# Kernel optimization log

Measured on AMD Instinct MI355X. Metric: run time of the kernel, lower is better.

The kernel has to match this reference:

```python
import jax, jax.numpy as jnp
import numpy as np

N = 100000      # n_heads + n_tails (graph nodes)
E = 1600000     # nnz of sparse adjacency A_in
D = 128         # in_dim == out_dim == embed_dim
LAMDA = 0.5
ALPHA = 0.1
LAYER = 1
LN_EPS = 1e-5
LEAKY_SLOPE = 0.01


def setup_inputs() -> dict:
    key = jax.random.key(0)
    ks = jax.random.split(key, 12)
    glorot = lambda k, shape: jax.random.uniform(
        k, shape, jnp.float32, -1.0, 1.0) * np.sqrt(6.0 / (shape[0] + shape[1]))
    stdv = 1.0 / np.sqrt(D)
    return {
        "ego_embeddings": jax.random.normal(ks[0], (N, D), jnp.float32),
        "h0": jax.random.normal(ks[1], (N, D), jnp.float32),  # all_layers[0]
        "vals": jax.random.uniform(ks[2], (E,), jnp.float32),
        "row": jax.random.randint(ks[3], (E,), 0, N, jnp.int32),
        "col": jax.random.randint(ks[4], (E,), 0, N, jnp.int32),
        # nn.Parameter weight (in_dim, in_dim), uniform(-stdv, stdv)
        "weight": jax.random.uniform(ks[5], (D, D), jnp.float32, -stdv, stdv),
        # linear_h0: embed_dim -> in_dim
        "w_h0": glorot(ks[6], (D, D)),
        "b_h0": jnp.zeros((D,), jnp.float32),
        # linear: in_dim -> out_dim
        "w_lin": glorot(ks[7], (D, D)),
        "b_lin": jnp.zeros((D,), jnp.float32),
        # LayerNorm(out_dim)
        "gamma": jnp.ones((D,), jnp.float32),
        "beta_ln": jnp.zeros((D,), jnp.float32),
    }


def _layernorm(x, g, b):
    mu = jnp.mean(x, axis=-1, keepdims=True)
    var = jnp.mean(jnp.square(x - mu), axis=-1, keepdims=True)
    return (x - mu) * jax.lax.rsqrt(var + LN_EPS) * g + b


def reference(ego_embeddings, h0, vals, weight, w_h0, b_h0, w_lin, b_lin,
              gamma, beta_ln, row, col):
    n = ego_embeddings.shape[0]
    # side_embeddings = A_in @ ego_embeddings  (sparse COO SpMM)
    msgs = vals[:, None] * ego_embeddings[col]          # [E, D] gather
    side = jax.ops.segment_sum(msgs, row, num_segments=n)
    # gcn aggregator
    hi = ego_embeddings + side
    # residual_connection with identity mapping (GCNII-style)
    h0p = h0 @ w_h0.T + b_h0
    residual = (1.0 - ALPHA) * hi + ALPHA * h0p
    beta = float(np.log(LAMDA / LAYER + 1.0))
    identity_mapping = (1.0 - beta) + beta * weight     # [D, D]
    emb = residual @ identity_mapping
    # linear + LeakyReLU
    emb = jax.nn.leaky_relu(emb @ w_lin.T + b_lin, LEAKY_SLOPE)
    # LayerNorm; dropout p=0 -> identity
    return _layernorm(emb, gamma, beta_ln)
```

## Files before the change

kernel.cpp:

```cpp
#include <hip/hip_runtime.h>

#define DD 128

__global__ void hist_k(const int* __restrict__ rowi, int* __restrict__ cnt, int E) {
  int e = blockIdx.x * 256 + threadIdx.x;
  if (e < E) atomicAdd(&cnt[rowi[e]], 1);
}

__global__ __launch_bounds__(256) void scan1_k(const int* __restrict__ cnt,
                                               int* __restrict__ bsum, int n) {
  __shared__ int red[256];
  int base = blockIdx.x * 1024 + threadIdx.x * 4;
  int s = 0;
  if (base + 3 < n) {
    int4 v = *(const int4*)(cnt + base);
    s = v.x + v.y + v.z + v.w;
  } else {
#pragma unroll
    for (int j = 0; j < 4; ++j) if (base + j < n) s += cnt[base + j];
  }
  red[threadIdx.x] = s;
  __syncthreads();
#pragma unroll
  for (int off = 128; off > 0; off >>= 1) {
    if (threadIdx.x < off) red[threadIdx.x] += red[threadIdx.x + off];
    __syncthreads();
  }
  if (threadIdx.x == 0) bsum[blockIdx.x] = red[0];
}

__global__ __launch_bounds__(256) void scan2_k(int* __restrict__ bsum, int nb) {
  __shared__ int part[256];
  int t = threadIdx.x;
  int v = (t < nb) ? bsum[t] : 0;
  part[t] = v;
  __syncthreads();
#pragma unroll
  for (int off = 1; off < 256; off <<= 1) {
    int u = (t >= off) ? part[t - off] : 0;
    __syncthreads();
    part[t] += u;
    __syncthreads();
  }
  if (t < nb) bsum[t] = part[t] - v;
}

__global__ __launch_bounds__(256) void scan3_k(const int* __restrict__ cnt,
                                               const int* __restrict__ bsum,
                                               int* __restrict__ rowptr,
                                               int* __restrict__ cursor, int n, int E) {
  __shared__ int tsum[256];
  int base = blockIdx.x * 1024 + threadIdx.x * 4;
  int v0 = 0, v1 = 0, v2 = 0, v3 = 0;
  if (base + 3 < n) {
    int4 v = *(const int4*)(cnt + base);
    v0 = v.x; v1 = v.y; v2 = v.z; v3 = v.w;
  } else {
    if (base + 0 < n) v0 = cnt[base + 0];
    if (base + 1 < n) v1 = cnt[base + 1];
    if (base + 2 < n) v2 = cnt[base + 2];
    if (base + 3 < n) v3 = cnt[base + 3];
  }
  int s = v0 + v1 + v2 + v3;
  tsum[threadIdx.x] = s;
  __syncthreads();
#pragma unroll
  for (int off = 1; off < 256; off <<= 1) {
    int u = (threadIdx.x >= off) ? tsum[threadIdx.x - off] : 0;
    __syncthreads();
    tsum[threadIdx.x] += u;
    __syncthreads();
  }
  int run = bsum[blockIdx.x] + tsum[threadIdx.x] - s;
  int p1 = run + v0, p2 = p1 + v1, p3 = p2 + v2;
  if (base + 3 < n) {
    *(int4*)(rowptr + base) = (int4){run, p1, p2, p3};
    *(int4*)(cursor + base) = (int4){run, p1, p2, p3};
  } else {
    if (base + 0 < n) { rowptr[base + 0] = run; cursor[base + 0] = run; }
    if (base + 1 < n) { rowptr[base + 1] = p1;  cursor[base + 1] = p1; }
    if (base + 2 < n) { rowptr[base + 2] = p2;  cursor[base + 2] = p2; }
    if (base + 3 < n) { rowptr[base + 3] = p3;  cursor[base + 3] = p3; }
  }
  if (blockIdx.x == 0 && threadIdx.x == 0) rowptr[n] = E;
}

__global__ void scatter_k(const int* __restrict__ rowi, const int* __restrict__ coli,
                          const float* __restrict__ vals, int* __restrict__ cursor,
                          int2* __restrict__ edgeS, int E) {
  int e = blockIdx.x * 256 + threadIdx.x;
  if (e < E) {
    int r = rowi[e];
    int p = atomicAdd(&cursor[r], 1);
    edgeS[p] = make_int2(coli[e], __float_as_int(vals[e]));
  }
}

__global__ void w2_k(const float* __restrict__ weight, const float* __restrict__ w_lin,
                     float* __restrict__ W2) {
  const float BETA = 0.40546510810816438f;
  int idx = blockIdx.x * 256 + threadIdx.x;
  int i = idx >> 7, j = idx & 127;
  const float* wi = weight + i * DD;
  const float* lj = w_lin + j * DD;
  float s = 0.f;
#pragma unroll 8
  for (int k = 0; k < DD; ++k) s = fmaf(fmaf(BETA, wi[k], 1.0f - BETA), lj[k], s);
  W2[idx] = s;
}

__global__ void wt_k(const float* __restrict__ W2, const float* __restrict__ w_h0,
                     const float* __restrict__ b_h0, const float* __restrict__ b_lin,
                     float* __restrict__ Wf, float* __restrict__ cvec) {
  int idx = blockIdx.x * 256 + threadIdx.x;
  if (idx < 16384) {
    Wf[idx] = 0.9f * W2[idx];
  } else if (idx < 32768) {
    int t = idx - 16384;
    int p = t >> 7, n = t & 127;
    float s = 0.f;
#pragma unroll 8
    for (int k = 0; k < DD; ++k) s = fmaf(w_h0[k * DD + p], W2[k * DD + n], s);
    Wf[(128 + p) * DD + n] = 0.1f * s;
  } else if (idx < 32896) {
    int n = idx - 32768;
    float s = 0.f;
    for (int k = 0; k < DD; ++k) s = fmaf(b_h0[k], W2[k * DD + n], s);
    cvec[n] = fmaf(0.1f, s, b_lin[n]);
  }
}

__global__ __launch_bounds__(256) void fused_k(
    const float* __restrict__ ego, const int2* __restrict__ edgeS,
    const int* __restrict__ rowptr, const float* __restrict__ h0,
    const float* __restrict__ Wf, const float* __restrict__ cvec,
    const float* __restrict__ gamma, const float* __restrict__ betaln,
    float* __restrict__ out, int n, int E) {
  __shared__ float lds[4][2048];
  int wave = threadIdx.x >> 6;
  int lane = threadIdx.x & 63;
  int half = lane >> 5;
  int q = lane & 31;
  float* xs = &lds[wave][0];
  int row0 = blockIdx.x * 32 + wave * 8;
  const float4* eg4 = (const float4*)ego;
  const float4* h4 = (const float4*)h0;

#pragma unroll
  for (int t = 0; t < 8; ++t) {
    int r = row0 + t;
    if (r >= n) r = n - 1;
    float4 acc;
    if (half == 0) acc = eg4[(size_t)r * 32 + q];
    else           acc = (float4){0.f, 0.f, 0.f, 0.f};
    float4 hrow = h4[(size_t)r * 32 + q];
    int beg = rowptr[r], end = rowptr[r + 1];
    int e = beg;
    for (; e + 8 <= end; e += 8) {
      int2 m0 = edgeS[e + 0 + half];
      int2 m1 = edgeS[e + 2 + half];
      int2 m2 = edgeS[e + 4 + half];
      int2 m3 = edgeS[e + 6 + half];
      float4 g0 = eg4[(size_t)m0.x * 32 + q];
      float4 g1 = eg4[(size_t)m1.x * 32 + q];
      float4 g2 = eg4[(size_t)m2.x * 32 + q];
      float4 g3 = eg4[(size_t)m3.x * 32 + q];
      float v0 = __int_as_float(m0.y), v1 = __int_as_float(m1.y);
      float v2 = __int_as_float(m2.y), v3 = __int_as_float(m3.y);
      acc.x = fmaf(v0, g0.x, acc.x); acc.y = fmaf(v0, g0.y, acc.y);
      acc.z = fmaf(v0, g0.z, acc.z); acc.w = fmaf(v0, g0.w, acc.w);
      acc.x = fmaf(v1, g1.x, acc.x); acc.y = fmaf(v1, g1.y, acc.y);
      acc.z = fmaf(v1, g1.z, acc.z); acc.w = fmaf(v1, g1.w, acc.w);
      acc.x = fmaf(v2, g2.x, acc.x); acc.y = fmaf(v2, g2.y, acc.y);
      acc.z = fmaf(v2, g2.z, acc.z); acc.w = fmaf(v2, g2.w, acc.w);
      acc.x = fmaf(v3, g3.x, acc.x); acc.y = fmaf(v3, g3.y, acc.y);
      acc.z = fmaf(v3, g3.z, acc.z); acc.w = fmaf(v3, g3.w, acc.w);
    }
    for (; e < end; e += 2) {
      int idx = e + half;
      bool ok = idx < end;
      int ci = ok ? idx : (E > idx ? idx : E - 1);
      if (ci >= E) ci = E - 1;
      int2 m = edgeS[ci];
      float v = ok ? __int_as_float(m.y) : 0.f;
      float4 g = eg4[(size_t)m.x * 32 + q];
      acc.x = fmaf(v, g.x, acc.x); acc.y = fmaf(v, g.y, acc.y);
      acc.z = fmaf(v, g.z, acc.z); acc.w = fmaf(v, g.w, acc.w);
    }
    acc.x += __shfl_xor(acc.x, 32, 64);
    acc.y += __shfl_xor(acc.y, 32, 64);
    acc.z += __shfl_xor(acc.z, 32, 64);
    acc.w += __shfl_xor(acc.w, 32, 64);
    if (half == 0) *(float4*)(xs + t * 256 + 4 * q) = acc;
    else           *(float4*)(xs + t * 256 + 128 + 4 * q) = hrow;
  }

  float acc0[8], acc1[8];
#pragma unroll
  for (int r = 0; r < 8; ++r) { acc0[r] = 0.f; acc1[r] = 0.f; }

  for (int kb = 0; kb < 64; ++kb) {
    int k = kb * 4;
    float wA0 = Wf[(k + 0) * DD + lane];
    float wA1 = Wf[(k + 1) * DD + lane];
    float wA2 = Wf[(k + 2) * DD + lane];
    float wA3 = Wf[(k + 3) * DD + lane];
    float wB0 = Wf[(k + 0) * DD + 64 + lane];
    float wB1 = Wf[(k + 1) * DD + 64 + lane];
    float wB2 = Wf[(k + 2) * DD + 64 + lane];
    float wB3 = Wf[(k + 3) * DD + 64 + lane];
#pragma unroll
    for (int r = 0; r < 8; ++r) {
      float4 xv = *(const float4*)(xs + r * 256 + k);
      acc0[r] = fmaf(xv.x, wA0, acc0[r]);
      acc0[r] = fmaf(xv.y, wA1, acc0[r]);
      acc0[r] = fmaf(xv.z, wA2, acc0[r]);
      acc0[r] = fmaf(xv.w, wA3, acc0[r]);
      acc1[r] = fmaf(xv.x, wB0, acc1[r]);
      acc1[r] = fmaf(xv.y, wB1, acc1[r]);
      acc1[r] = fmaf(xv.z, wB2, acc1[r]);
      acc1[r] = fmaf(xv.w, wB3, acc1[r]);
    }
  }

  float cb0 = cvec[lane], cb1 = cvec[64 + lane];
#pragma unroll
  for (int r = 0; r < 8; ++r) {
    float t0 = acc0[r] + cb0;
    t0 = (t0 > 0.f) ? t0 : 0.01f * t0;
    float t1 = acc1[r] + cb1;
    t1 = (t1 > 0.f) ? t1 : 0.01f * t1;
    xs[r * 132 + lane] = t0;
    xs[r * 132 + 64 + lane] = t1;
  }

  int r = lane >> 3, p = lane & 7;
  const float* base = xs + r * 132 + p * 16;
  float4 va[4];
  float s = 0.f, qq = 0.f;
#pragma unroll
  for (int j = 0; j < 4; ++j) {
    float4 t = *(const float4*)(base + j * 4);
    va[j] = t;
    s += t.x + t.y + t.z + t.w;
    qq = fmaf(t.x, t.x, qq);
    qq = fmaf(t.y, t.y, qq);
    qq = fmaf(t.z, t.z, qq);
    qq = fmaf(t.w, t.w, qq);
  }
  s += __shfl_xor(s, 1, 64);
  s += __shfl_xor(s, 2, 64);
  s += __shfl_xor(s, 4, 64);
  qq += __shfl_xor(qq, 1, 64);
  qq += __shfl_xor(qq, 2, 64);
  qq += __shfl_xor(qq, 4, 64);
  float mean = s * (1.f / 128.f);
  float var = fmaf(qq, 1.f / 128.f, -mean * mean);
  float rstd = rsqrtf(var + 1e-5f);

  int orow = row0 + r;
  if (orow < n) {
    float* op = out + (size_t)orow * DD + p * 16;
    const float* gp = gamma + p * 16;
    const float* bp = betaln + p * 16;
#pragma unroll
    for (int j = 0; j < 4; ++j) {
      float4 g = *(const float4*)(gp + j * 4);
      float4 b = *(const float4*)(bp + j * 4);
      float4 o;
      o.x = fmaf((va[j].x - mean) * rstd, g.x, b.x);
      o.y = fmaf((va[j].y - mean) * rstd, g.y, b.y);
      o.z = fmaf((va[j].z - mean) * rstd, g.z, b.z);
      o.w = fmaf((va[j].w - mean) * rstd, g.w, b.w);
      *(float4*)(op + j * 4) = o;
    }
  }
}

extern "C" void kernel_launch(void* const* d_in, const int* in_sizes, int n_in,
                              void* d_out, int out_size, void* d_ws, size_t ws_size,
                              hipStream_t stream) {
  const float* ego    = (const float*)d_in[0];
  const float* h0     = (const float*)d_in[1];
  const float* vals   = (const float*)d_in[2];
  const int*   rowi   = (const int*)d_in[3];
  const int*   coli   = (const int*)d_in[4];
  const float* weight = (const float*)d_in[5];
  const float* w_h0   = (const float*)d_in[6];
  const float* b_h0   = (const float*)d_in[7];
  const float* w_lin  = (const float*)d_in[8];
  const float* b_lin  = (const float*)d_in[9];
  const float* gamma  = (const float*)d_in[10];
  const float* betaln = (const float*)d_in[11];

  const int N = in_sizes[0] / DD;
  const int E = in_sizes[2];
  const int NB = (N + 1023) / 1024;

  char* p = (char*)d_ws;
  auto carve = [&](size_t bytes) {
    char* q = p;
    p += (bytes + 255) & ~(size_t)255;
    return q;
  };
  int*   cnt    = (int*)carve((size_t)N * 4);
  int*   rowptr = (int*)carve((size_t)(N + 1) * 4);
  int*   cursor = (int*)carve((size_t)(N + 1) * 4);
  int*   bsum   = (int*)carve((size_t)256 * 4);
  int2*  edgeS  = (int2*)carve((size_t)E * 8);
  float* W2     = (float*)carve(16384 * 4);
  float* Wf     = (float*)carve(32768 * 4);
  float* cvec   = (float*)carve(128 * 4);
  (void)n_in; (void)out_size; (void)ws_size;

  float* outf = (float*)d_out;

  hipMemsetAsync(cnt, 0, (size_t)N * 4, stream);
  hist_k<<<(E + 255) / 256, 256, 0, stream>>>(rowi, cnt, E);
  w2_k<<<64, 256, 0, stream>>>(weight, w_lin, W2);
  scan1_k<<<NB, 256, 0, stream>>>(cnt, bsum, N);
  scan2_k<<<1, 256, 0, stream>>>(bsum, NB);
  scan3_k<<<NB, 256, 0, stream>>>(cnt, bsum, rowptr, cursor, N, E);
  scatter_k<<<(E + 255) / 256, 256, 0, stream>>>(rowi, coli, vals, cursor, edgeS, E);
  wt_k<<<129, 256, 0, stream>>>(W2, w_h0, b_h0, b_lin, Wf, cvec);
  fused_k<<<(N + 31) / 32, 256, 0, stream>>>(ego, edgeS, rowptr, h0, Wf, cvec,
                                             gamma, betaln, outf, N, E);
}
```

Measured before the change: 427.6 us.

## Halve rows per wave and broadcast edge indices via wave shuffles

Result: faster. 394.6 us (-7.7%).

```diff
diff --git a/kernel.cpp b/kernel.cpp
--- a/kernel.cpp
+++ b/kernel.cpp
@@ -135,58 +135,70 @@
     const int* __restrict__ rowptr, const float* __restrict__ h0,
     const float* __restrict__ Wf, const float* __restrict__ cvec,
     const float* __restrict__ gamma, const float* __restrict__ betaln,
-    float* __restrict__ out, int n, int E) {
-  __shared__ float lds[4][2048];
+    float* __restrict__ out, int n) {
+  __shared__ float lds[4][1024];
   int wave = threadIdx.x >> 6;
   int lane = threadIdx.x & 63;
   int half = lane >> 5;
   int q = lane & 31;
   float* xs = &lds[wave][0];
-  int row0 = blockIdx.x * 32 + wave * 8;
+  int row0 = blockIdx.x * 16 + wave * 4;
   const float4* eg4 = (const float4*)ego;
   const float4* h4 = (const float4*)h0;
 
 #pragma unroll
-  for (int t = 0; t < 8; ++t) {
+  for (int t = 0; t < 4; ++t) {
     int r = row0 + t;
     if (r >= n) r = n - 1;
-    float4 acc;
-    if (half == 0) acc = eg4[(size_t)r * 32 + q];
-    else           acc = (float4){0.f, 0.f, 0.f, 0.f};
+    float4 acc = (half == 0) ? eg4[(size_t)r * 32 + q] : (float4){0.f, 0.f, 0.f, 0.f};
+    float4 acc2 = {0.f, 0.f, 0.f, 0.f};
     float4 hrow = h4[(size_t)r * 32 + q];
     int beg = rowptr[r], end = rowptr[r + 1];
-    int e = beg;
-    for (; e + 8 <= end; e += 8) {
-      int2 m0 = edgeS[e + 0 + half];
-      int2 m1 = edgeS[e + 2 + half];
-      int2 m2 = edgeS[e + 4 + half];
-      int2 m3 = edgeS[e + 6 + half];
-      float4 g0 = eg4[(size_t)m0.x * 32 + q];
-      float4 g1 = eg4[(size_t)m1.x * 32 + q];
-      float4 g2 = eg4[(size_t)m2.x * 32 + q];
-      float4 g3 = eg4[(size_t)m3.x * 32 + q];
-      float v0 = __int_as_float(m0.y), v1 = __int_as_float(m1.y);
-      float v2 = __int_as_float(m2.y), v3 = __int_as_float(m3.y);
-      acc.x = fmaf(v0, g0.x, acc.x); acc.y = fmaf(v0, g0.y, acc.y);
-      acc.z = fmaf(v0, g0.z, acc.z); acc.w = fmaf(v0, g0.w, acc.w);
-      acc.x = fmaf(v1, g1.x, acc.x); acc.y = fmaf(v1, g1.y, acc.y);
-      acc.z = fmaf(v1, g1.z, acc.z); acc.w = fmaf(v1, g1.w, acc.w);
-      acc.x = fmaf(v2, g2.x, acc.x); acc.y = fmaf(v2, g2.y, acc.y);
-      acc.z = fmaf(v2, g2.z, acc.z); acc.w = fmaf(v2, g2.w, acc.w);
-      acc.x = fmaf(v3, g3.x, acc.x); acc.y = fmaf(v3, g3.y, acc.y);
-      acc.z = fmaf(v3, g3.z, acc.z); acc.w = fmaf(v3, g3.w, acc.w);
+    for (int cb = beg; cb < end; cb += 64) {
+      int cnt = end - cb;
+      if (cnt > 64) cnt = 64;
+      int mcol = 0;
+      float mval = 0.f;
+      if (lane < cnt) {
+        int2 m = edgeS[cb + lane];
+        mcol = m.x;
+        mval = __int_as_float(m.y);
+      }
+      int npair = (cnt + 1) >> 1;
+      int j = 0;
+      for (; j + 4 <= npair; j += 4) {
+        int i0 = 2 * j + half;
+        int c0 = __shfl(mcol, i0, 64);
+        int c1 = __shfl(mcol, i0 + 2, 64);
+        int c2 = __shfl(mcol, i0 + 4, 64);
+        int c3 = __shfl(mcol, i0 + 6, 64);
+        float v0 = __shfl(mval, i0, 64);
+        float v1 = __shfl(mval, i0 + 2, 64);
+        float v2 = __shfl(mval, i0 + 4, 64);
+        float v3 = __shfl(mval, i0 + 6, 64);
+        float4 g0 = eg4[(size_t)c0 * 32 + q];
+        float4 g1 = eg4[(size_t)c1 * 32 + q];
+        float4 g2 = eg4[(size_t)c2 * 32 + q];
+        float4 g3 = eg4[(size_t)c3 * 32 + q];
+        acc.x  = fmaf(v0, g0.x, acc.x);  acc.y  = fmaf(v0, g0.y, acc.y);
+        acc.z  = fmaf(v0, g0.z, acc.z);  acc.w  = fmaf(v0, g0.w, acc.w);
+        acc2.x = fmaf(v1, g1.x, acc2.x); acc2.y = fmaf(v1, g1.y, acc2.y);
+        acc2.z = fmaf(v1, g1.z, acc2.z); acc2.w = fmaf(v1, g1.w, acc2.w);
+        acc.x  = fmaf(v2, g2.x, acc.x);  acc.y  = fmaf(v2, g2.y, acc.y);
+        acc.z  = fmaf(v2, g2.z, acc.z);  acc.w  = fmaf(v2, g2.w, acc.w);
+        acc2.x = fmaf(v3, g3.x, acc2.x); acc2.y = fmaf(v3, g3.y, acc2.y);
+        acc2.z = fmaf(v3, g3.z, acc2.z); acc2.w = fmaf(v3, g3.w, acc2.w);
+      }
+      for (; j < npair; ++j) {
+        int i0 = 2 * j + half;
+        int c0 = __shfl(mcol, i0, 64);
+        float v0 = __shfl(mval, i0, 64);
+        float4 g0 = eg4[(size_t)c0 * 32 + q];
+        acc.x = fmaf(v0, g0.x, acc.x); acc.y = fmaf(v0, g0.y, acc.y);
+        acc.z = fmaf(v0, g0.z, acc.z); acc.w = fmaf(v0, g0.w, acc.w);
+      }
     }
-    for (; e < end; e += 2) {
-      int idx = e + half;
-      bool ok = idx < end;
-      int ci = ok ? idx : (E > idx ? idx : E - 1);
-      if (ci >= E) ci = E - 1;
-      int2 m = edgeS[ci];
-      float v = ok ? __int_as_float(m.y) : 0.f;
-      float4 g = eg4[(size_t)m.x * 32 + q];
-      acc.x = fmaf(v, g.x, acc.x); acc.y = fmaf(v, g.y, acc.y);
-      acc.z = fmaf(v, g.z, acc.z); acc.w = fmaf(v, g.w, acc.w);
-    }
+    acc.x += acc2.x; acc.y += acc2.y; acc.z += acc2.z; acc.w += acc2.w;
     acc.x += __shfl_xor(acc.x, 32, 64);
     acc.y += __shfl_xor(acc.y, 32, 64);
     acc.z += __shfl_xor(acc.z, 32, 64);
@@ -195,9 +207,9 @@
     else           *(float4*)(xs + t * 256 + 128 + 4 * q) = hrow;
   }
 
-  float acc0[8], acc1[8];
-#pragma unroll
-  for (int r = 0; r < 8; ++r) { acc0[r] = 0.f; acc1[r] = 0.f; }
+  float acc0[4], acc1[4];
+#pragma unroll
+  for (int r = 0; r < 4; ++r) { acc0[r] = 0.f; acc1[r] = 0.f; }
 
   for (int kb = 0; kb < 64; ++kb) {
     int k = kb * 4;
@@ -210,7 +222,7 @@
     float wB2 = Wf[(k + 2) * DD + 64 + lane];
     float wB3 = Wf[(k + 3) * DD + 64 + lane];
 #pragma unroll
-    for (int r = 0; r < 8; ++r) {
+    for (int r = 0; r < 4; ++r) {
       float4 xv = *(const float4*)(xs + r * 256 + k);
       acc0[r] = fmaf(xv.x, wA0, acc0[r]);
       acc0[r] = fmaf(xv.y, wA1, acc0[r]);
@@ -225,7 +237,7 @@
 
   float cb0 = cvec[lane], cb1 = cvec[64 + lane];
 #pragma unroll
-  for (int r = 0; r < 8; ++r) {
+  for (int r = 0; r < 4; ++r) {
     float t0 = acc0[r] + cb0;
     t0 = (t0 > 0.f) ? t0 : 0.01f * t0;
     float t1 = acc1[r] + cb1;
@@ -234,12 +246,12 @@
     xs[r * 132 + 64 + lane] = t1;
   }
 
-  int r = lane >> 3, p = lane & 7;
-  const float* base = xs + r * 132 + p * 16;
-  float4 va[4];
+  int r = lane >> 4, p = lane & 15;
+  const float* base = xs + r * 132 + p * 8;
+  float4 va[2];
   float s = 0.f, qq = 0.f;
 #pragma unroll
-  for (int j = 0; j < 4; ++j) {
+  for (int j = 0; j < 2; ++j) {
     float4 t = *(const float4*)(base + j * 4);
     va[j] = t;
     s += t.x + t.y + t.z + t.w;
@@ -251,20 +263,22 @@
   s += __shfl_xor(s, 1, 64);
   s += __shfl_xor(s, 2, 64);
   s += __shfl_xor(s, 4, 64);
+  s += __shfl_xor(s, 8, 64);
   qq += __shfl_xor(qq, 1, 64);
   qq += __shfl_xor(qq, 2, 64);
   qq += __shfl_xor(qq, 4, 64);
+  qq += __shfl_xor(qq, 8, 64);
   float mean = s * (1.f / 128.f);
   float var = fmaf(qq, 1.f / 128.f, -mean * mean);
   float rstd = rsqrtf(var + 1e-5f);
 
   int orow = row0 + r;
   if (orow < n) {
-    float* op = out + (size_t)orow * DD + p * 16;
-    const float* gp = gamma + p * 16;
-    const float* bp = betaln + p * 16;
-#pragma unroll
-    for (int j = 0; j < 4; ++j) {
+    float* op = out + (size_t)orow * DD + p * 8;
+    const float* gp = gamma + p * 8;
+    const float* bp = betaln + p * 8;
+#pragma unroll
+    for (int j = 0; j < 2; ++j) {
       float4 g = *(const float4*)(gp + j * 4);
       float4 b = *(const float4*)(bp + j * 4);
       float4 o;
@@ -323,6 +337,6 @@
   scan3_k<<<NB, 256, 0, stream>>>(cnt, bsum, rowptr, cursor, N, E);
   scatter_k<<<(E + 255) / 256, 256, 0, stream>>>(rowi, coli, vals, cursor, edgeS, E);
   wt_k<<<129, 256, 0, stream>>>(W2, w_h0, b_h0, b_lin, Wf, cvec);
-  fused_k<<<(N + 31) / 32, 256, 0, stream>>>(ego, edgeS, rowptr, h0, Wf, cvec,
-                                             gamma, betaln, outf, N, E);
-}
+  fused_k<<<(N + 15) / 16, 256, 0, stream>>>(ego, edgeS, rowptr, h0, Wf, cvec,
+                                             gamma, betaln, outf, N);
+}
```
